# Kernel optimization log

Measured on AMD Instinct MI355X. Metric: run time of the kernel, lower is better.

The kernel has to match this reference:

```python
import jax, jax.numpy as jnp
import numpy as np

B, K, V = 256, 8, 50257
T = B * K
PLACEHOLDER = -1


def setup_inputs() -> dict:
    key = jax.random.key(0)
    ks = jax.random.split(key, 7)
    num_draft_tokens = jax.random.randint(ks[0], (B,), 0, K + 1).astype(jnp.int32)
    draft_token_ids = jax.random.randint(ks[1], (T,), 0, V).astype(jnp.int32)
    dp = jax.random.uniform(ks[2], (T, V), jnp.float32) + 1e-3
    draft_probs = dp / dp.sum(-1, keepdims=True)
    tp = jax.random.uniform(ks[3], (T, V), jnp.float32) + 1e-3
    target_probs = tp / tp.sum(-1, keepdims=True)
    bonus_token_ids = jax.random.randint(ks[4], (B, 1), 0, V).astype(jnp.int32)
    uniform_samples = jax.random.uniform(ks[5], (T,), jnp.float32)
    resample_uniforms = jax.random.uniform(ks[6], (B,), jnp.float32)
    return {
        "draft_token_ids": draft_token_ids,
        "num_draft_tokens": num_draft_tokens,
        "draft_probs": draft_probs,
        "target_probs": target_probs,
        "bonus_token_ids": bonus_token_ids,
        "uniform_samples": uniform_samples,
        "resample_uniforms": resample_uniforms,
        "max_spec_len": K,
    }


def reference(draft_token_ids, num_draft_tokens, draft_probs, target_probs,
              bonus_token_ids, uniform_samples, resample_uniforms, max_spec_len):
    # Packed layout: sequence b owns token rows [starts[b], starts[b]+n[b]).
    n = num_draft_tokens.astype(jnp.int32)              # [B]
    cu = jnp.cumsum(n)                                  # [B]
    starts = cu - n                                     # [B] exclusive cumsum
    total = draft_token_ids.shape[0]
    ks = jnp.arange(max_spec_len, dtype=jnp.int32)      # [K]

    tok_idx = starts[:, None] + ks[None, :]             # [B,K] packed row index
    valid = ks[None, :] < n[:, None]                    # [B,K]
    idx = jnp.clip(tok_idx, 0, total - 1)

    dtok = draft_token_ids[idx]                         # [B,K] draft token ids
    p_draft = jnp.maximum(draft_probs[idx, dtok], 1e-10)
    p_target = target_probs[idx, dtok]
    u = uniform_samples[idx]
    accept_prob = jnp.minimum(1.0, p_target / p_draft)
    accept = (u < accept_prob) & valid                  # [B,K]

    # Leading run of accepted drafts (the torch loop breaks at first rejection).
    run = jnp.cumprod(accept.astype(jnp.int32), axis=1) # [B,K]
    num_acc = run.sum(axis=1).astype(jnp.int32)         # [B] accepted draft count
    all_accepted = num_acc == n                         # [B]

    # Recovered token at the first rejected position (inverse-CDF multinomial).
    rej_pos = jnp.clip(num_acc, 0, max_spec_len - 1)
    rej_idx = jnp.clip(starts + rej_pos, 0, total - 1)  # [B]
    t_row = target_probs[rej_idx]                       # [B,V]
    d_row = draft_probs[rej_idx]                        # [B,V]
    adjusted = jnp.maximum(t_row - d_row, 0.0)
    s = adjusted.sum(-1, keepdims=True)
    probs = jnp.where(s > 1e-10, adjusted / jnp.maximum(s, 1e-30), t_row)
    cdf = jnp.cumsum(probs, axis=-1)
    recovered = jnp.sum(cdf < resample_uniforms[:, None], axis=-1)
    recovered = jnp.clip(recovered, 0, probs.shape[-1] - 1).astype(jnp.int32)

    # Assemble outputs: accepted drafts, then recovered (reject) or bonus (all-accept).
    final_tok = jnp.where(all_accepted, bonus_token_ids[:, 0], recovered)  # [B]
    pos = jnp.arange(max_spec_len + 1, dtype=jnp.int32)                    # [K+1]
    dtok_pad = jnp.pad(dtok, ((0, 0), (0, 1)))                             # [B,K+1]
    out = jnp.where(pos[None, :] < num_acc[:, None], dtok_pad,
                    jnp.where(pos[None, :] == num_acc[:, None], final_tok[:, None],
                              PLACEHOLDER)).astype(jnp.int32)

    num_accepted = num_acc + 1                          # always one extra token emitted
    accepted_counts = num_acc
    recovered_counts = (~all_accepted).astype(jnp.int32)
    bonus_counts = all_accepted.astype(jnp.int32)
    return out, num_accepted, accepted_counts, recovered_counts, bonus_counts
```

## Files before the change

### kernel.cpp

```cpp
#include <hip/hip_runtime.h>

#define PLACEHOLDER (-1)

constexpr int MAXK = 16;

__global__ __launch_bounds__(1024)
void k1_accept(const int* __restrict__ draft_token_ids,
               const int* __restrict__ num_draft_tokens,
               const float* __restrict__ draft_probs,
               const float* __restrict__ target_probs,
               const int* __restrict__ bonus_token_ids,
               const float* __restrict__ uniform_samples,
               int* __restrict__ out,
               int* __restrict__ num_accepted,
               int* __restrict__ accepted_counts,
               int* __restrict__ recovered_counts,
               int* __restrict__ bonus_counts,
               int* __restrict__ ws_info,
               int B, int K, int V, int T)
{
    __shared__ int s_scan[1024];
    const int b = threadIdx.x;
    const int n = (b < B) ? num_draft_tokens[b] : 0;
    s_scan[b] = n;
    __syncthreads();
    for (int off = 1; off < B; off <<= 1) {
        int v = 0;
        if (b >= off) v = s_scan[b - off];
        __syncthreads();
        s_scan[b] += v;
        __syncthreads();
    }
    if (b >= B) return;
    const int start = s_scan[b] - n;

    int toks[MAXK];
    #pragma unroll
    for (int k = 0; k < MAXK; k++)
        if (k < K && k < n) toks[k] = draft_token_ids[start + k];

    float pd[MAXK], pt[MAXK], uu[MAXK];
    #pragma unroll
    for (int k = 0; k < MAXK; k++) {
        if (k < K && k < n) {
            const long long row = (long long)(start + k) * (long long)V;
            pd[k] = draft_probs[row + toks[k]];
            pt[k] = target_probs[row + toks[k]];
            uu[k] = uniform_samples[start + k];
        }
    }

    int num_acc = 0;
    bool running = true;
    #pragma unroll
    for (int k = 0; k < MAXK; k++) {
        if (k < K && k < n && running) {
            const float d  = fmaxf(pd[k], 1e-10f);
            const float ap = fminf(1.0f, pt[k] / d);
            if (uu[k] < ap) num_acc++; else running = false;
        }
    }
    const bool all_acc = (num_acc == n);

    int* orow = out + b * (K + 1);
    #pragma unroll
    for (int p = 0; p < MAXK + 1; p++) {
        if (p <= K) {
            int val = PLACEHOLDER;
            if (p < num_acc)        val = toks[p];
            else if (p == num_acc)  val = all_acc ? bonus_token_ids[b] : PLACEHOLDER;
            orow[p] = val;
        }
    }

    num_accepted[b]     = num_acc + 1;
    accepted_counts[b]  = num_acc;
    recovered_counts[b] = all_acc ? 0 : 1;
    bonus_counts[b]     = all_acc ? 1 : 0;

    int rej_pos = num_acc; if (rej_pos > K - 1) rej_pos = K - 1;
    int rej_row = start + rej_pos;
    if (rej_row > T - 1) rej_row = T - 1;
    if (rej_row < 0)     rej_row = 0;
    ws_info[2 * b]     = rej_row;
    ws_info[2 * b + 1] = all_acc ? -1 : num_acc;
}

#define K2_BLOCK 1024
#define K2_C     4
#define K2_TILE  (K2_BLOCK * K2_C)
#define MAX_TILES 64

__global__ __launch_bounds__(K2_BLOCK)
void k2_resample(const float* __restrict__ draft_probs,
                 const float* __restrict__ target_probs,
                 const float* __restrict__ resample_uniforms,
                 const int* __restrict__ ws_info,
                 int* __restrict__ out,
                 int B, int K, int V)
{
    const int b    = blockIdx.x;
    const int slot = ws_info[2 * b + 1];
    if (slot < 0) return;
    const int row  = ws_info[2 * b];
    const float* __restrict__ trow = target_probs + (long long)row * (long long)V;
    const float* __restrict__ drow = draft_probs  + (long long)row * (long long)V;
    const float u = resample_uniforms[b];

    const int tid  = threadIdx.x;
    const int lane = tid & 63;
    const int wave = tid >> 6;

    __shared__ float s_adj[MAX_TILES];
    __shared__ float s_t[MAX_TILES];
    __shared__ float s_wa[16];
    __shared__ float s_wt[16];
    __shared__ float s_w[16];
    __shared__ int   s_cnt[16];

    const int NT = (V + K2_TILE - 1) / K2_TILE;

    for (int t = 0; t < NT; t++) {
        const int base = t * K2_TILE;
        float ta[K2_C], da[K2_C];
        #pragma unroll
        for (int c = 0; c < K2_C; c++) {
            const int idx = base + c * K2_BLOCK + tid;
            const bool ok = idx < V;
            ta[c] = ok ? trow[idx] : 0.0f;
            da[c] = ok ? drow[idx] : 0.0f;
        }
        float aa = 0.0f, at = 0.0f;
        #pragma unroll
        for (int c = 0; c < K2_C; c++) {
            aa += fmaxf(ta[c] - da[c], 0.0f);
            at += ta[c];
        }
        #pragma unroll
        for (int off = 32; off; off >>= 1) {
            aa += __shfl_down(aa, off, 64);
            at += __shfl_down(at, off, 64);
        }
        if (lane == 0) { s_wa[wave] = aa; s_wt[wave] = at; }
        __syncthreads();
        if (tid == 0) {
            float sa = 0.0f, st = 0.0f;
            for (int w = 0; w < 16; w++) { sa += s_wa[w]; st += s_wt[w]; }
            s_adj[t] = sa; s_t[t] = st;
        }
        __syncthreads();
    }

    float s = 0.0f;
    for (int t = 0; t < NT; t++) s += s_adj[t];
    const bool  use_adj = (s > 1e-10f);
    const float thresh  = use_adj ? u * s : u;
    const float* sums   = use_adj ? s_adj : s_t;

    int tc = -1; float base = 0.0f;
    for (int t = 0; t < NT; t++) {
        const float ns = base + sums[t];
        if (ns >= thresh) { tc = t; break; }
        base = ns;
    }

    if (tc < 0) {
        if (tid == 0) out[b * (K + 1) + slot] = V - 1;
        return;
    }

    int cnt = 0;
    float run = base;
    for (int c = 0; c < K2_C; c++) {
        const int idx = tc * K2_TILE + c * K2_BLOCK + tid;
        const bool ok = idx < V;
        float v = 0.0f;
        if (ok) {
            const float tv = trow[idx];
            v = use_adj ? fmaxf(tv - drow[idx], 0.0f) : tv;
        }
        float x = v;
        #pragma unroll
        for (int off = 1; off < 64; off <<= 1) {
            const float y = __shfl_up(x, off, 64);
            if (lane >= off) x += y;
        }
        if (lane == 63) s_w[wave] = x;
        __syncthreads();
        float wbase = 0.0f, chunk = 0.0f;
        for (int w = 0; w < 16; w++) {
            const float ws = s_w[w];
            if (w < wave) wbase += ws;
            chunk += ws;
        }
        const float incl = run + wbase + x;
        if (ok && incl < thresh) cnt++;
        run += chunk;
        __syncthreads();
    }
    #pragma unroll
    for (int off = 32; off; off >>= 1) cnt += __shfl_down(cnt, off, 64);
    if (lane == 0) s_cnt[wave] = cnt;
    __syncthreads();
    if (tid == 0) {
        int tot = 0;
        for (int w = 0; w < 16; w++) tot += s_cnt[w];
        int recovered = tc * K2_TILE + tot;
        if (recovered > V - 1) recovered = V - 1;
        out[b * (K + 1) + slot] = recovered;
    }
}

extern "C" void kernel_launch(void* const* d_in, const int* in_sizes, int n_in,
                              void* d_out, int out_size, void* d_ws, size_t ws_size,
                              hipStream_t stream)
{
    const int*   draft_token_ids   = (const int*)  d_in[0];
    const int*   num_draft_tokens  = (const int*)  d_in[1];
    const float* draft_probs       = (const float*)d_in[2];
    const float* target_probs      = (const float*)d_in[3];
    const int*   bonus_token_ids   = (const int*)  d_in[4];
    const float* uniform_samples   = (const float*)d_in[5];
    const float* resample_uniforms = (const float*)d_in[6];

    const int T = in_sizes[0];
    const int B = in_sizes[1];
    const int V = (int)((long long)in_sizes[2] / (long long)T);
    const int K = T / B;

    int* out              = (int*)d_out;
    int* num_accepted     = out + B * (K + 1);
    int* accepted_counts  = num_accepted + B;
    int* recovered_counts = accepted_counts + B;
    int* bonus_counts     = recovered_counts + B;
    int* ws_info          = (int*)d_ws;

    k1_accept<<<1, B, 0, stream>>>(draft_token_ids, num_draft_tokens,
                                   draft_probs, target_probs, bonus_token_ids,
                                   uniform_samples, out, num_accepted,
                                   accepted_counts, recovered_counts,
                                   bonus_counts, ws_info, B, K, V, T);

    k2_resample<<<B, K2_BLOCK, 0, stream>>>(draft_probs, target_probs,
                                            resample_uniforms, ws_info, out,
                                            B, K, V);
}
```

Baseline: 644.0 us.

## Fuse acceptance and resampling kernels into one per-sequence block kernel

The single-block acceptance kernel is removed. Each resampling block now computes its own sequence's prefix offset and acceptance with one wave, using a ballot to find the first rejection, so one launch and the global workspace handoff go away. The per-tile reduction also drops its two barriers per tile: partial sums go into per-tile shared slots and are reduced once after the loop. The cost is that every block redundantly reads num_draft_tokens and runs a serial wave-0 phase before the bandwidth-bound resample pass. Lanes are assumed to cover K (K up to 64).

```diff
diff --git a/kernel.cpp b/kernel.cpp
--- a/kernel.cpp
+++ b/kernel.cpp
@@ -2,89 +2,6 @@
 
 #define PLACEHOLDER (-1)
 
-constexpr int MAXK = 16;
-
-__global__ __launch_bounds__(1024)
-void k1_accept(const int* __restrict__ draft_token_ids,
-               const int* __restrict__ num_draft_tokens,
-               const float* __restrict__ draft_probs,
-               const float* __restrict__ target_probs,
-               const int* __restrict__ bonus_token_ids,
-               const float* __restrict__ uniform_samples,
-               int* __restrict__ out,
-               int* __restrict__ num_accepted,
-               int* __restrict__ accepted_counts,
-               int* __restrict__ recovered_counts,
-               int* __restrict__ bonus_counts,
-               int* __restrict__ ws_info,
-               int B, int K, int V, int T)
-{
-    __shared__ int s_scan[1024];
-    const int b = threadIdx.x;
-    const int n = (b < B) ? num_draft_tokens[b] : 0;
-    s_scan[b] = n;
-    __syncthreads();
-    for (int off = 1; off < B; off <<= 1) {
-        int v = 0;
-        if (b >= off) v = s_scan[b - off];
-        __syncthreads();
-        s_scan[b] += v;
-        __syncthreads();
-    }
-    if (b >= B) return;
-    const int start = s_scan[b] - n;
-
-    int toks[MAXK];
-    #pragma unroll
-    for (int k = 0; k < MAXK; k++)
-        if (k < K && k < n) toks[k] = draft_token_ids[start + k];
-
-    float pd[MAXK], pt[MAXK], uu[MAXK];
-    #pragma unroll
-    for (int k = 0; k < MAXK; k++) {
-        if (k < K && k < n) {
-            const long long row = (long long)(start + k) * (long long)V;
-            pd[k] = draft_probs[row + toks[k]];
-            pt[k] = target_probs[row + toks[k]];
-            uu[k] = uniform_samples[start + k];
-        }
-    }
-
-    int num_acc = 0;
-    bool running = true;
-    #pragma unroll
-    for (int k = 0; k < MAXK; k++) {
-        if (k < K && k < n && running) {
-            const float d  = fmaxf(pd[k], 1e-10f);
-            const float ap = fminf(1.0f, pt[k] / d);
-            if (uu[k] < ap) num_acc++; else running = false;
-        }
-    }
-    const bool all_acc = (num_acc == n);
-
-    int* orow = out + b * (K + 1);
-    #pragma unroll
-    for (int p = 0; p < MAXK + 1; p++) {
-        if (p <= K) {
-            int val = PLACEHOLDER;
-            if (p < num_acc)        val = toks[p];
-            else if (p == num_acc)  val = all_acc ? bonus_token_ids[b] : PLACEHOLDER;
-            orow[p] = val;
-        }
-    }
-
-    num_accepted[b]     = num_acc + 1;
-    accepted_counts[b]  = num_acc;
-    recovered_counts[b] = all_acc ? 0 : 1;
-    bonus_counts[b]     = all_acc ? 1 : 0;
-
-    int rej_pos = num_acc; if (rej_pos > K - 1) rej_pos = K - 1;
-    int rej_row = start + rej_pos;
-    if (rej_row > T - 1) rej_row = T - 1;
-    if (rej_row < 0)     rej_row = 0;
-    ws_info[2 * b]     = rej_row;
-    ws_info[2 * b + 1] = all_acc ? -1 : num_acc;
-}
 
 #define K2_BLOCK 1024
 #define K2_C     4
@@ -92,32 +9,94 @@
 #define MAX_TILES 64
 
 __global__ __launch_bounds__(K2_BLOCK)
-void k2_resample(const float* __restrict__ draft_probs,
-                 const float* __restrict__ target_probs,
-                 const float* __restrict__ resample_uniforms,
-                 const int* __restrict__ ws_info,
-                 int* __restrict__ out,
-                 int B, int K, int V)
+void fused_rejection(const int* __restrict__ draft_token_ids,
+                     const int* __restrict__ num_draft_tokens,
+                     const float* __restrict__ draft_probs,
+                     const float* __restrict__ target_probs,
+                     const int* __restrict__ bonus_token_ids,
+                     const float* __restrict__ uniform_samples,
+                     const float* __restrict__ resample_uniforms,
+                     int* __restrict__ out,
+                     int* __restrict__ num_accepted,
+                     int* __restrict__ accepted_counts,
+                     int* __restrict__ recovered_counts,
+                     int* __restrict__ bonus_counts,
+                     int B, int K, int V, int T)
 {
     const int b    = blockIdx.x;
-    const int slot = ws_info[2 * b + 1];
+    const int tid  = threadIdx.x;
+    const int lane = tid & 63;
+    const int wave = tid >> 6;
+
+    __shared__ float s_wa[MAX_TILES * 16];
+    __shared__ float s_wt[MAX_TILES * 16];
+    __shared__ float s_adj[MAX_TILES];
+    __shared__ float s_t[MAX_TILES];
+    __shared__ float s_w[16];
+    __shared__ int   s_cnt[16];
+    __shared__ int   s_info[2];
+
+    if (wave == 0) {
+        int acc = 0, nb = 0;
+        for (int i = lane; i < B; i += 64) {
+            const int v = num_draft_tokens[i];
+            if (i < b)  acc += v;
+            if (i == b) nb  = v;
+        }
+        #pragma unroll
+        for (int off = 32; off; off >>= 1) {
+            acc += __shfl_down(acc, off, 64);
+            nb  += __shfl_down(nb,  off, 64);
+        }
+        const int start = __shfl(acc, 0, 64);
+        const int n     = __shfl(nb,  0, 64);
+
+        int  tok = 0;
+        bool accept_lane = false;
+        if (lane < K && lane < n) {
+            const int r = start + lane;
+            tok = draft_token_ids[r];
+            const long long ro = (long long)r * (long long)V;
+            const float d = fmaxf(draft_probs[ro + tok], 1e-10f);
+            const float t = target_probs[ro + tok];
+            const float u = uniform_samples[r];
+            accept_lane = (u < fminf(1.0f, t / d));
+        }
+        const unsigned long long mask  = __ballot(accept_lane);
+        const unsigned long long valid = (n >= 64) ? ~0ull : ((1ull << n) - 1ull);
+        const unsigned long long m2    = (~mask) & valid;
+        const int  num_acc = m2 ? (int)(__ffsll(m2) - 1) : n;
+        const bool all_acc = (num_acc == n);
+
+        if (lane <= K) {
+            int val = PLACEHOLDER;
+            if (lane < num_acc)                  val = tok;
+            else if (lane == num_acc && all_acc) val = bonus_token_ids[b];
+            out[b * (K + 1) + lane] = val;
+        }
+        if (lane == 0) {
+            num_accepted[b]     = num_acc + 1;
+            accepted_counts[b]  = num_acc;
+            recovered_counts[b] = all_acc ? 0 : 1;
+            bonus_counts[b]     = all_acc ? 1 : 0;
+
+            int rej_pos = num_acc; if (rej_pos > K - 1) rej_pos = K - 1;
+            int rej_row = start + rej_pos;
+            if (rej_row > T - 1) rej_row = T - 1;
+            if (rej_row < 0)     rej_row = 0;
+            s_info[0] = rej_row;
+            s_info[1] = all_acc ? -1 : num_acc;
+        }
+    }
+    __syncthreads();
+
+    const int slot = s_info[1];
     if (slot < 0) return;
-    const int row  = ws_info[2 * b];
+    const int row  = s_info[0];
+
     const float* __restrict__ trow = target_probs + (long long)row * (long long)V;
     const float* __restrict__ drow = draft_probs  + (long long)row * (long long)V;
     const float u = resample_uniforms[b];
-
-    const int tid  = threadIdx.x;
-    const int lane = tid & 63;
-    const int wave = tid >> 6;
-
-    __shared__ float s_adj[MAX_TILES];
-    __shared__ float s_t[MAX_TILES];
-    __shared__ float s_wa[16];
-    __shared__ float s_wt[16];
-    __shared__ float s_w[16];
-    __shared__ int   s_cnt[16];
-
     const int NT = (V + K2_TILE - 1) / K2_TILE;
 
     for (int t = 0; t < NT; t++) {
@@ -141,15 +120,22 @@
             aa += __shfl_down(aa, off, 64);
             at += __shfl_down(at, off, 64);
         }
-        if (lane == 0) { s_wa[wave] = aa; s_wt[wave] = at; }
-        __syncthreads();
-        if (tid == 0) {
-            float sa = 0.0f, st = 0.0f;
-            for (int w = 0; w < 16; w++) { sa += s_wa[w]; st += s_wt[w]; }
-            s_adj[t] = sa; s_t[t] = st;
-        }
-        __syncthreads();
-    }
+        if (lane == 0) {
+            s_wa[t * 16 + wave] = aa;
+            s_wt[t * 16 + wave] = at;
+        }
+    }
+    __syncthreads();
+    if (tid < NT) {
+        float sa = 0.0f, st = 0.0f;
+        for (int w = 0; w < 16; w++) {
+            sa += s_wa[tid * 16 + w];
+            st += s_wt[tid * 16 + w];
+        }
+        s_adj[tid] = sa;
+        s_t[tid]   = st;
+    }
+    __syncthreads();
 
     float s = 0.0f;
     for (int t = 0; t < NT; t++) s += s_adj[t];
@@ -233,15 +219,10 @@
     int* accepted_counts  = num_accepted + B;
     int* recovered_counts = accepted_counts + B;
     int* bonus_counts     = recovered_counts + B;
-    int* ws_info          = (int*)d_ws;
-
-    k1_accept<<<1, B, 0, stream>>>(draft_token_ids, num_draft_tokens,
-                                   draft_probs, target_probs, bonus_token_ids,
-                                   uniform_samples, out, num_accepted,
-                                   accepted_counts, recovered_counts,
-                                   bonus_counts, ws_info, B, K, V, T);
-
-    k2_resample<<<B, K2_BLOCK, 0, stream>>>(draft_probs, target_probs,
-                                            resample_uniforms, ws_info, out,
-                                            B, K, V);
+
+    fused_rejection<<<B, K2_BLOCK, 0, stream>>>(
+        draft_token_ids, num_draft_tokens, draft_probs, target_probs,
+        bonus_token_ids, uniform_samples, resample_uniforms,
+        out, num_accepted, accepted_counts, recovered_counts, bonus_counts,
+        B, K, V, T);
 }
```

After: 627.9 us. 1.03x faster.
